# Performance work log

Measured on AMD Instinct MI355X. Metric: run time of the kernel, lower is better.

## Reference

```python
import jax, jax.numpy as jnp
import numpy as np


def _lstm_dir(xg, m, Whh, reverse):
    # xg: (T,B,4H) precomputed x@Wih.T + b ; m: (T,B) float mask
    T, B, G = xg.shape
    H = G // 4
    if reverse:
        xg = xg[::-1]
        m = m[::-1]

    def step(carry, inp):
        h, c = carry
        xg_t, m_t = inp
        gates = xg_t + h @ Whh.T
        i, f, g, o = jnp.split(gates, 4, axis=-1)  # torch gate order i,f,g,o
        i = jax.nn.sigmoid(i); f = jax.nn.sigmoid(f)
        g = jnp.tanh(g); o = jax.nn.sigmoid(o)
        c_new = f * c + i * g
        h_new = o * jnp.tanh(c_new)
        mt = m_t[:, None]
        h = mt * h_new + (1.0 - mt) * h
        c = mt * c_new + (1.0 - mt) * c
        return (h, c), h * mt  # zero outputs at padding like pad_packed_sequence

    init = (jnp.zeros((B, H), xg.dtype), jnp.zeros((B, H), xg.dtype))
    _, hs = jax.lax.scan(step, init, (xg, m))
    if reverse:
        hs = hs[::-1]
    return hs  # (T,B,H)


def _viterbi(feats, mask_f, transitions):
    # feats: (B,T,K) emissions incl. START/STOP rows; mask_f: (B,T) float
    B, T, K = feats.shape
    START, STOP = K - 2, K - 1
    part0 = transitions[START][None, :] + feats[:, 0, :]  # (B,K)
    ident = jnp.broadcast_to(jnp.arange(K)[None, :], (B, K))

    def step(part, inp):
        feat_t, m_t = inp
        cur = part[:, :, None] + transitions[None, :, :] + feat_t[:, None, :]
        new = cur.max(axis=1)
        bp = cur.argmax(axis=1)
        mb = (m_t > 0)[:, None]
        part = jnp.where(mb, new, part)        # carry partition through padding
        bp = jnp.where(mb, bp, ident)          # identity pointer at padding
        return part, bp

    part, bps = jax.lax.scan(
        step, part0, (feats[:, 1:].transpose(1, 0, 2), mask_f[:, 1:].T))
    final = part + transitions[:, STOP][None, :]
    best_score = final.max(axis=-1)            # (B,)
    last_tag = final.argmax(axis=-1)           # (B,)

    def back(tag, bp_t):
        prev = jnp.take_along_axis(bp_t, tag[:, None], axis=1)[:, 0]
        return prev, prev

    _, prevs = jax.lax.scan(back, last_tag, bps, reverse=True)  # (T-1,B)
    decode = jnp.concatenate([prevs, last_tag[None, :]], axis=0).T  # (B,T)
    return best_score, decode


def setup_inputs() -> dict:
    key = jax.random.key(0)
    ks = jax.random.split(key, 16)
    B, T, E, H = 256, 200, 256, 256
    Vc, Vf, n_labels = 10000, 100, 50
    K = n_labels + 2
    lengths = jnp.sort(jax.random.randint(ks[0], (B,), 1, T + 1))[::-1]
    lengths = lengths.at[0].set(T)
    mask = jnp.arange(T)[None, :] < lengths[:, None]
    s = 0.1
    trans = s * jax.random.normal(ks[11], (K, K), jnp.float32)
    trans = trans.at[:, K - 2].set(-10000.0)  # nothing transitions to START
    trans = trans.at[K - 1, :].set(-10000.0)  # nothing transitions from STOP
    return {
        'batch_input': jax.random.randint(ks[1], (B, T), 0, Vc),
        'batch_feature': jax.random.randint(ks[2], (B, T), 0, Vf),
        'batch_len': lengths,
        'batch_recover': jnp.arange(B),
        'mask': mask,
        'char_table': s * jax.random.normal(ks[3], (Vc, E), jnp.float32),
        'feat_table': 1.0 + s * jax.random.normal(ks[4], (Vf, E), jnp.float32),
        'Wih_f': s * jax.random.normal(ks[5], (4 * H, E), jnp.float32),
        'Whh_f': s * jax.random.normal(ks[6], (4 * H, H), jnp.float32),
        'b_f': s * jax.random.normal(ks[7], (4 * H,), jnp.float32),
        'Wih_b': s * jax.random.normal(ks[8], (4 * H, E), jnp.float32),
        'Whh_b': s * jax.random.normal(ks[9], (4 * H, H), jnp.float32),
        'b_b': s * jax.random.normal(ks[10], (4 * H,), jnp.float32),
        'W_tag': s * jax.random.normal(ks[12], (K, 2 * H), jnp.float32),
        'b_tag': s * jax.random.normal(ks[13], (K,), jnp.float32),
        'transitions': trans,
    }


def reference(batch_input, batch_feature, batch_len, batch_recover, mask,
              char_table, feat_table, Wih_f, Whh_f, b_f, Wih_b, Whh_b, b_b,
              W_tag, b_tag, transitions):
    # embeddings (dropout is identity at inference)
    emb = char_table[batch_input] * feat_table[batch_feature]  # (B,T,E)
    x = emb.transpose(1, 0, 2)                                 # (T,B,E)
    m = mask.astype(x.dtype).T                                 # (T,B)
    xg_f = jnp.einsum('tbe,ge->tbg', x, Wih_f) + b_f
    xg_b = jnp.einsum('tbe,ge->tbg', x, Wih_b) + b_b
    h_f = _lstm_dir(xg_f, m, Whh_f, reverse=False)
    h_b = _lstm_dir(xg_b, m, Whh_b, reverse=True)
    lstm_out = jnp.concatenate([h_f, h_b], axis=-1).transpose(1, 0, 2)  # (B,T,2H)
    feats = jnp.einsum('bth,kh->btk', lstm_out, W_tag) + b_tag          # (B,T,K)
    best_score, decode = _viterbi(feats, mask.astype(feats.dtype), transitions)
    decode = decode * mask.astype(decode.dtype)
    return best_score, decode
```

## Files before the change

kernel.cpp:

```cpp
#include <hip/hip_runtime.h>
#include <math.h>

#define T_ 200
#define WROW 284
#define SMEM_FLOATS (128 * WROW + 16 * WROW)
#define SMEM_BYTES (SMEM_FLOATS * 4)

typedef float f32x2 __attribute__((ext_vector_type(2)));

__device__ __forceinline__ float fsig(float x) {
  return 1.f / (1.f + __expf(-x));
}
__device__ __forceinline__ float ftanh(float x) {
  return 1.f - 2.f / (__expf(2.f * x) + 1.f);
}

__global__ __launch_bounds__(256) void xg_gemm(
    const int* __restrict__ bin, const int* __restrict__ bfe,
    const int* __restrict__ blen,
    const float* __restrict__ ctab, const float* __restrict__ ftab,
    const float* __restrict__ wih, const float* __restrict__ bias,
    float* __restrict__ xgslot, int t0, int sgn) {
  const int m0 = blockIdx.x * 128;
  const int rloc = m0 >> 8;
  const int t_blk = t0 + sgn * rloc;
  if (t_blk >= blen[m0 & 255]) return;

  __shared__ float As[32][140];
  __shared__ float Bs[32][132];
  const int tid = threadIdx.x;
  const int n0 = blockIdx.y * 128;
  const int mm = tid & 15;
  const int nn = tid >> 4;

  const int ra = tid & 127;
  const int ka = (tid >> 7) << 4;

  const int bcol = (m0 + ra) & 255;
  const float* cr = ctab + ((size_t)bin[bcol * T_ + t_blk] << 8);
  const float* fr = ftab + ((size_t)bfe[bcol * T_ + t_blk] << 8);
  const float* br = wih + (size_t)(n0 + ra) * 256;
  const int cwa = ra + ((ra >> 5) << 2);

  f32x2 acc[8][4];
  #pragma unroll
  for (int i = 0; i < 8; ++i)
    #pragma unroll
    for (int j = 0; j < 4; ++j) acc[i][j] = (f32x2){0.f, 0.f};

  const int am0 = mm * 8 + ((mm >> 2) << 2);
  const int bn0 = nn * 8;

  for (int ks = 0; ks < 256; ks += 32) {
    float4 c4[4], f4v[4], b4[4];
    #pragma unroll
    for (int w = 0; w < 4; ++w) {
      c4[w]  = *(const float4*)(cr + ks + ka + w * 4);
      f4v[w] = *(const float4*)(fr + ks + ka + w * 4);
      b4[w]  = *(const float4*)(br + ks + ka + w * 4);
    }
    __syncthreads();
    #pragma unroll
    for (int w = 0; w < 4; ++w) {
      int kk = ka + w * 4;
      As[kk + 0][cwa] = c4[w].x * f4v[w].x;
      As[kk + 1][cwa] = c4[w].y * f4v[w].y;
      As[kk + 2][cwa] = c4[w].z * f4v[w].z;
      As[kk + 3][cwa] = c4[w].w * f4v[w].w;
      Bs[kk + 0][ra] = b4[w].x;
      Bs[kk + 1][ra] = b4[w].y;
      Bs[kk + 2][ra] = b4[w].z;
      Bs[kk + 3][ra] = b4[w].w;
    }
    __syncthreads();
    #pragma unroll 4
    for (int k = 0; k < 32; ++k) {
      float4 a0 = *(const float4*)&As[k][am0];
      float4 a1 = *(const float4*)&As[k][am0 + 4];
      float4 b0 = *(const float4*)&Bs[k][bn0];
      float4 b1 = *(const float4*)&Bs[k][bn0 + 4];
      float am[8] = {a0.x, a0.y, a0.z, a0.w, a1.x, a1.y, a1.z, a1.w};
      f32x2 bp[4] = {{b0.x, b0.y}, {b0.z, b0.w}, {b1.x, b1.y}, {b1.z, b1.w}};
      #pragma unroll
      for (int i = 0; i < 8; ++i) {
        f32x2 av = {am[i], am[i]};
        #pragma unroll
        for (int j = 0; j < 4; ++j)
          acc[i][j] = __builtin_elementwise_fma(av, bp[j], acc[i][j]);
      }
    }
  }

  float4 bv0 = *(const float4*)(bias + n0 + bn0);
  float4 bv1 = *(const float4*)(bias + n0 + bn0 + 4);
  #pragma unroll
  for (int i = 0; i < 8; ++i) {
    int row = m0 + mm * 8 + i;
    float4 o0, o1;
    o0.x = acc[i][0].x + bv0.x; o0.y = acc[i][0].y + bv0.y;
    o0.z = acc[i][1].x + bv0.z; o0.w = acc[i][1].y + bv0.w;
    o1.x = acc[i][2].x + bv1.x; o1.y = acc[i][2].y + bv1.y;
    o1.z = acc[i][3].x + bv1.z; o1.w = acc[i][3].y + bv1.w;
    *(float4*)(xgslot + (size_t)row * 1024 + n0 + bn0) = o0;
    *(float4*)(xgslot + (size_t)row * 1024 + n0 + bn0 + 4) = o1;
  }
}

__global__ __launch_bounds__(512, 1) void lstm_chunk(
    const float* __restrict__ xgf, const float* __restrict__ xgb,
    const float* __restrict__ whf, const float* __restrict__ whb,
    const int* __restrict__ blen,
    float* __restrict__ hst, float* __restrict__ cst,
    float* __restrict__ hout, unsigned* __restrict__ bar,
    int s0, int nsteps) {
  extern __shared__ float smem[];
  float* wlds = smem;
  float* hlds = smem + 128 * WROW;

  const int bc = blockIdx.x, js = blockIdx.y, dir = blockIdx.z;
  const int tid = threadIdx.x;
  const int ks = tid & 7;
  const int bg = (tid >> 3) & 3;
  const int rg = tid >> 5;
  const int grp = dir * 16 + bc;
  const float* wh = dir ? whb : whf;
  const float* xgp = dir ? xgb : xgf;

  #pragma unroll
  for (int i = 0; i < 16; ++i) {
    int f = tid + i * 512;
    int prow = f >> 6;
    int k = (f & 63) << 2;
    int g = (prow >> 1) & 3, u = prow & 1, rgs = prow >> 3;
    int jg = js * 32 + rgs * 2 + u;
    float4 v = *(const float4*)(wh + ((size_t)(g * 256 + jg)) * 256 + k);
    *(float4*)&wlds[prow * WROW + k + ((k >> 5) << 2)] = v;
  }

  const int bl_th = bg * 4 + (ks & 3);
  const int b_th = bc * 16 + bl_th;
  const int u_th = ks >> 2;
  const int jth = js * 32 + rg * 2 + u_th;
  const int cjth = jth + ((jth >> 5) << 2);
  const int len_th = blen[b_th];
  float c0 = cst[((size_t)dir * 256 + b_th) * 256 + jth];

  float xq[4];
  #pragma unroll
  for (int g = 0; g < 4; ++g)
    xq[g] = xgp[(size_t)b_th * 1024 + g * 256 + jth];

  __syncthreads();

  for (int r = 0; r < nsteps; ++r) {
    const int s = s0 + r;
    const int tt = dir ? (199 - s) : s;
    const int rslot = s & 1, wslot = 1 - rslot;

    const float* hsrc = hst + (((size_t)(rslot * 2 + dir)) * 256 + bc * 16) * 256;
    {
      const int f0 = tid, f1 = tid + 512;
      const int b0i = f0 >> 6, k0 = (f0 & 63) << 2;
      const int b1i = f1 >> 6, k1 = (f1 & 63) << 2;
      const float* p0 = hsrc + (b0i << 8) + k0;
      const float* p1 = hsrc + (b1i << 8) + k1;
      float4 v0, v1;
      asm volatile(
          "global_load_dwordx4 %0, %2, off sc1\n\t"
          "global_load_dwordx4 %1, %3, off sc1\n\t"
          "s_waitcnt vmcnt(0)"
          : "=&v"(v0), "=&v"(v1)
          : "v"(p0), "v"(p1)
          : "memory");
      *(float4*)&hlds[b0i * WROW + k0 + ((k0 >> 5) << 2)] = v0;
      *(float4*)&hlds[b1i * WROW + k1 + ((k1 >> 5) << 2)] = v1;
    }
    __syncthreads();

    float xqn[4];
    const int rn = (r + 1 < nsteps) ? (r + 1) : r;
    #pragma unroll
    for (int g = 0; g < 4; ++g)
      xqn[g] = xgp[((size_t)rn * 256 + b_th) * 1024 + g * 256 + jth];

    f32x2 acc2[8][4];
    #pragma unroll
    for (int i = 0; i < 8; ++i)
      #pragma unroll
      for (int bb = 0; bb < 4; ++bb) acc2[i][bb] = (f32x2){0.f, 0.f};

    #pragma unroll
    for (int kq = 0; kq < 8; ++kq) {
      const int col = ks * 36 + kq * 4;
      float4 h4[4];
      #pragma unroll
      for (int bb = 0; bb < 4; ++bb)
        h4[bb] = *(const float4*)&hlds[(bg * 4 + bb) * WROW + col];
      f32x2 hlo[4], hhi[4];
      #pragma unroll
      for (int bb = 0; bb < 4; ++bb) {
        hlo[bb] = (f32x2){h4[bb].x, h4[bb].y};
        hhi[bb] = (f32x2){h4[bb].z, h4[bb].w};
      }
      #pragma unroll
      for (int i = 0; i < 8; ++i) {
        float4 w4 = *(const float4*)&wlds[(rg * 8 + i) * WROW + col];
        f32x2 wlo = (f32x2){w4.x, w4.y};
        f32x2 whi = (f32x2){w4.z, w4.w};
        #pragma unroll
        for (int bb = 0; bb < 4; ++bb) {
          acc2[i][bb] = __builtin_elementwise_fma(wlo, hlo[bb], acc2[i][bb]);
          acc2[i][bb] = __builtin_elementwise_fma(whi, hhi[bb], acc2[i][bb]);
        }
      }
    }

    float acc[8][4];
    #pragma unroll
    for (int i = 0; i < 8; ++i)
      #pragma unroll
      for (int bb = 0; bb < 4; ++bb)
        acc[i][bb] = acc2[i][bb].x + acc2[i][bb].y;

    const int bit0 = ks & 1, bit1 = (ks >> 1) & 1;
    float fin[8];
    #pragma unroll
    for (int i = 0; i < 8; ++i) {
      float k0 = bit0 ? acc[i][1] : acc[i][0];
      float s0v = bit0 ? acc[i][0] : acc[i][1];
      float k1 = bit0 ? acc[i][3] : acc[i][2];
      float s1v = bit0 ? acc[i][2] : acc[i][3];
      float r0 = k0 + __shfl_xor(s0v, 1);
      float r1 = k1 + __shfl_xor(s1v, 1);
      float k2 = bit1 ? r1 : r0;
      float s2v = bit1 ? r0 : r1;
      float r2 = k2 + __shfl_xor(s2v, 2);
      fin[i] = r2 + __shfl_xor(r2, 4);
    }

    float gi = fsig((u_th ? fin[1] : fin[0]) + xq[0]);
    float gf = fsig((u_th ? fin[3] : fin[2]) + xq[1]);
    float gg = ftanh((u_th ? fin[5] : fin[4]) + xq[2]);
    float go = fsig((u_th ? fin[7] : fin[6]) + xq[3]);
    float cn = gf * c0 + gi * gg;
    float hn = go * ftanh(cn);
    const bool mk = tt < len_th;
    if (mk) c0 = cn;
    float hold = hlds[bl_th * WROW + cjth];
    float hsv = mk ? hn : hold;
    __hip_atomic_store(
        hst + (((size_t)(wslot * 2 + dir)) * 256 + b_th) * 256 + jth,
        hsv, __ATOMIC_RELAXED, __HIP_MEMORY_SCOPE_AGENT);

    asm volatile("s_waitcnt vmcnt(0)" ::: "memory");
    __syncthreads();
    if (tid == 0)
      __hip_atomic_fetch_add(&bar[grp * 32], 1u, __ATOMIC_RELAXED,
                             __HIP_MEMORY_SCOPE_AGENT);
    hout[(((size_t)dir * 200 + tt) * 256 + b_th) * 256 + jth] = mk ? hn : 0.f;
    if (tid == 0) {
      const unsigned tgt = 8u * (unsigned)(s + 1);
      while (__hip_atomic_load(&bar[grp * 32], __ATOMIC_RELAXED,
                               __HIP_MEMORY_SCOPE_AGENT) < tgt) {}
    }
    __syncthreads();

    #pragma unroll
    for (int g = 0; g < 4; ++g) xq[g] = xqn[g];
  }

  cst[((size_t)dir * 256 + b_th) * 256 + jth] = c0;
}

__global__ __launch_bounds__(256) void feats_kernel(
    const float* __restrict__ h_out, const float* __restrict__ wtag,
    const float* __restrict__ btag, float* __restrict__ feats) {
  __shared__ float hcat[32][512];
  const int t = blockIdx.x, bc = blockIdx.y;
  const int tid = threadIdx.x;
  const float* hf = h_out + (((size_t)0 * 200 + t) * 256 + bc * 32) * 256;
  const float* hb = h_out + (((size_t)1 * 200 + t) * 256 + bc * 32) * 256;
  for (int i = tid; i < 2048; i += 256) {
    int row = i >> 6, c4 = (i & 63) << 2;
    *(float4*)&hcat[row][c4] = *(const float4*)(hf + (size_t)row * 256 + c4);
    *(float4*)&hcat[row][256 + c4] = *(const float4*)(hb + (size_t)row * 256 + c4);
  }
  __syncthreads();
  const int kk = tid & 63;
  const int bg = tid >> 6;
  if (kk < 52) {
    f32x2 acc2[8];
    #pragma unroll
    for (int i = 0; i < 8; ++i) acc2[i] = (f32x2){0.f, 0.f};
    const float* wr = wtag + (size_t)kk * 512;
    for (int jq = 0; jq < 128; ++jq) {
      float4 wv = *(const float4*)(wr + jq * 4);
      f32x2 wlo = (f32x2){wv.x, wv.y};
      f32x2 whi = (f32x2){wv.z, wv.w};
      #pragma unroll
      for (int bi = 0; bi < 8; ++bi) {
        float4 hv = *(const float4*)&hcat[bg * 8 + bi][jq * 4];
        f32x2 hlo = (f32x2){hv.x, hv.y};
        f32x2 hhi = (f32x2){hv.z, hv.w};
        acc2[bi] = __builtin_elementwise_fma(wlo, hlo, acc2[bi]);
        acc2[bi] = __builtin_elementwise_fma(whi, hhi, acc2[bi]);
      }
    }
    float bv = btag[kk];
    #pragma unroll
    for (int bi = 0; bi < 8; ++bi)
      feats[(size_t)(bc * 32 + bg * 8 + bi) * 10400 + t * 52 + kk] =
          acc2[bi].x + acc2[bi].y + bv;
  }
}

__global__ __launch_bounds__(64) void viterbi_kernel(
    const float* __restrict__ feats, const float* __restrict__ trans,
    const int* __restrict__ blen, float* __restrict__ out) {
  __shared__ float flds[10400];
  __shared__ float pl[56];
  __shared__ unsigned char bp[199 * 52];

  const int b = blockIdx.x;
  const int lane = threadIdx.x;
  const int kk = (lane < 52) ? lane : 0;
  const float* fb = feats + (size_t)b * 10400;
  const int len = blen[b];

  for (int i = lane; i < 2600; i += 64)
    *(float4*)&flds[i * 4] = *(const float4*)(fb + i * 4);

  float trc[52];
  #pragma unroll
  for (int j = 0; j < 52; ++j) trc[j] = trans[j * 52 + kk];
  __syncthreads();

  float part = trans[50 * 52 + kk] + flds[kk];
  if (lane < 52) pl[lane] = part;

  for (int t = 1; t < 200; ++t) {
    const float ftk = flds[t * 52 + kk];
    float pa[52];
    #pragma unroll
    for (int q = 0; q < 13; ++q) {
      float4 v = *(const float4*)&pl[q * 4];
      pa[q * 4 + 0] = v.x; pa[q * 4 + 1] = v.y;
      pa[q * 4 + 2] = v.z; pa[q * 4 + 3] = v.w;
    }
    float mv0 = -1e30f, mv1 = -1e30f, mv2 = -1e30f, mv3 = -1e30f;
    int mj0 = 0, mj1 = 13, mj2 = 26, mj3 = 39;
    #pragma unroll
    for (int q = 0; q < 13; ++q) {
      float c0v = (pa[q] + trc[q]) + ftk;
      if (c0v > mv0) { mv0 = c0v; mj0 = q; }
      float c1v = (pa[13 + q] + trc[13 + q]) + ftk;
      if (c1v > mv1) { mv1 = c1v; mj1 = 13 + q; }
      float c2v = (pa[26 + q] + trc[26 + q]) + ftk;
      if (c2v > mv2) { mv2 = c2v; mj2 = 26 + q; }
      float c3v = (pa[39 + q] + trc[39 + q]) + ftk;
      if (c3v > mv3) { mv3 = c3v; mj3 = 39 + q; }
    }
    float mv = mv0; int mj = mj0;
    if (mv1 > mv) { mv = mv1; mj = mj1; }
    if (mv2 > mv) { mv = mv2; mj = mj2; }
    if (mv3 > mv) { mv = mv3; mj = mj3; }
    const bool m = t < len;
    if (lane < 52) {
      bp[(t - 1) * 52 + lane] = (unsigned char)(m ? mj : lane);
      if (m) { part = mv; pl[lane] = mv; }
    }
  }

  float fin = (lane < 52) ? (part + trans[lane * 52 + 51]) : -1e30f;
  int bi = lane;
  #pragma unroll
  for (int off = 32; off; off >>= 1) {
    float ov = __shfl_down(fin, off);
    int oi = __shfl_down(bi, off);
    if (ov > fin || (ov == fin && oi < bi)) { fin = ov; bi = oi; }
  }
  if (lane == 0) {
    out[b] = fin;
    int tag = bi;
    float* dec = out + 256 + (size_t)b * 200;
    dec[199] = (199 < len) ? (float)tag : 0.f;
    for (int i = 198; i >= 0; --i) {
      tag = bp[i * 52 + tag];
      dec[i] = (i < len) ? (float)tag : 0.f;
    }
  }
}

extern "C" void kernel_launch(void* const* d_in, const int* in_sizes, int n_in,
                              void* d_out, int out_size, void* d_ws, size_t ws_size,
                              hipStream_t stream) {
  const int*   bin  = (const int*)d_in[0];
  const int*   bfe  = (const int*)d_in[1];
  const int*   blen = (const int*)d_in[2];
  const float* ctab = (const float*)d_in[5];
  const float* ftab = (const float*)d_in[6];
  const float* wihf = (const float*)d_in[7];
  const float* whhf = (const float*)d_in[8];
  const float* bf   = (const float*)d_in[9];
  const float* wihb = (const float*)d_in[10];
  const float* whhb = (const float*)d_in[11];
  const float* bb   = (const float*)d_in[12];
  const float* wtag = (const float*)d_in[13];
  const float* btag = (const float*)d_in[14];
  const float* trn  = (const float*)d_in[15];

  (void)hipFuncSetAttribute(reinterpret_cast<const void*>(lstm_chunk),
                            hipFuncAttributeMaxDynamicSharedMemorySize,
                            SMEM_BYTES);

  const size_t FIXED_F = 29271040;
  size_t ws_f = ws_size / sizeof(float);
  int C = 1;
  const int cands[10] = {50, 40, 25, 20, 10, 8, 5, 4, 2, 1};
  for (int u = 0; u < 10; ++u) {
    if (FIXED_F + (size_t)2 * cands[u] * 262144 <= ws_f) { C = cands[u]; break; }
  }

  float* ws  = (float*)d_ws;
  float* xgf = ws;
  float* xgb = xgf + (size_t)C * 262144;
  float* hst = xgb + (size_t)C * 262144;
  float* cst = hst + 262144;
  float* hout = cst + 131072;
  float* fts  = hout + 26214400;
  unsigned* bar = (unsigned*)(fts + 2662400);
  float* out  = (float*)d_out;

  hipMemsetAsync(hst, 0, (size_t)(262144 + 131072) * sizeof(float), stream);
  hipMemsetAsync(bar, 0, 1024 * sizeof(unsigned), stream);

  const int nchunks = 200 / C;
  for (int c = 0; c < nchunks; ++c) {
    xg_gemm<<<dim3(2 * C, 8), 256, 0, stream>>>(bin, bfe, blen, ctab, ftab,
                                                wihf, bf, xgf, c * C, 1);
    xg_gemm<<<dim3(2 * C, 8), 256, 0, stream>>>(bin, bfe, blen, ctab, ftab,
                                                wihb, bb, xgb, 199 - c * C, -1);
    lstm_chunk<<<dim3(16, 8, 2), 512, SMEM_BYTES, stream>>>(
        xgf, xgb, whhf, whhb, blen, hst, cst, hout, bar, c * C, C);
  }
  feats_kernel<<<dim3(200, 8), 256, 0, stream>>>(hout, wtag, btag, fts);
  viterbi_kernel<<<256, 64, 0, stream>>>(fts, trn, blen, out);
}
```

Measured before the change: 2.243 ms.

## Prefetch LSTM weights, use DPP reductions, skip padded steps in feats and Viterbi

Inside the LSTM recurrent step, the W tile loads for the next k-slice are software-pipelined into registers, and two of the cross-lane shuffles are replaced with DPP quad permutes. The feats kernel now exits early for timesteps past the first sequence length of each 32-row batch chunk. The Viterbi kernel loads only the valid prefix, runs only up to each sequence's length, and backtracks only over valid positions. Skipping feats blocks assumes lengths are sorted descending within each batch chunk, and the prefetch raises register pressure in the LSTM kernel.

```diff
diff --git a/kernel.cpp b/kernel.cpp
--- a/kernel.cpp
+++ b/kernel.cpp
@@ -13,6 +13,14 @@
 }
 __device__ __forceinline__ float ftanh(float x) {
   return 1.f - 2.f / (__expf(2.f * x) + 1.f);
+}
+__device__ __forceinline__ float dpp_xor1(float x) {
+  return __int_as_float(__builtin_amdgcn_update_dpp(
+      0, __float_as_int(x), 0xB1, 0xF, 0xF, true));
+}
+__device__ __forceinline__ float dpp_xor2(float x) {
+  return __int_as_float(__builtin_amdgcn_update_dpp(
+      0, __float_as_int(x), 0x4E, 0xF, 0xF, true));
 }
 
 __global__ __launch_bounds__(256) void xg_gemm(
@@ -189,6 +197,11 @@
       #pragma unroll
       for (int bb = 0; bb < 4; ++bb) acc2[i][bb] = (f32x2){0.f, 0.f};
 
+    float4 w4c[8];
+    #pragma unroll
+    for (int i = 0; i < 8; ++i)
+      w4c[i] = *(const float4*)&wlds[(rg * 8 + i) * WROW + ks * 36];
+
     #pragma unroll
     for (int kq = 0; kq < 8; ++kq) {
       const int col = ks * 36 + kq * 4;
@@ -196,6 +209,12 @@
       #pragma unroll
       for (int bb = 0; bb < 4; ++bb)
         h4[bb] = *(const float4*)&hlds[(bg * 4 + bb) * WROW + col];
+      float4 w4n[8];
+      if (kq < 7) {
+        #pragma unroll
+        for (int i = 0; i < 8; ++i)
+          w4n[i] = *(const float4*)&wlds[(rg * 8 + i) * WROW + col + 4];
+      }
       f32x2 hlo[4], hhi[4];
       #pragma unroll
       for (int bb = 0; bb < 4; ++bb) {
@@ -204,15 +223,18 @@
       }
       #pragma unroll
       for (int i = 0; i < 8; ++i) {
-        float4 w4 = *(const float4*)&wlds[(rg * 8 + i) * WROW + col];
-        f32x2 wlo = (f32x2){w4.x, w4.y};
-        f32x2 whi = (f32x2){w4.z, w4.w};
+        f32x2 wlo = (f32x2){w4c[i].x, w4c[i].y};
+        f32x2 whi = (f32x2){w4c[i].z, w4c[i].w};
         #pragma unroll
         for (int bb = 0; bb < 4; ++bb) {
           acc2[i][bb] = __builtin_elementwise_fma(wlo, hlo[bb], acc2[i][bb]);
           acc2[i][bb] = __builtin_elementwise_fma(whi, hhi[bb], acc2[i][bb]);
         }
       }
+      if (kq < 7) {
+        #pragma unroll
+        for (int i = 0; i < 8; ++i) w4c[i] = w4n[i];
+      }
     }
 
     float acc[8][4];
@@ -230,11 +252,11 @@
       float s0v = bit0 ? acc[i][0] : acc[i][1];
       float k1 = bit0 ? acc[i][3] : acc[i][2];
       float s1v = bit0 ? acc[i][2] : acc[i][3];
-      float r0 = k0 + __shfl_xor(s0v, 1);
-      float r1 = k1 + __shfl_xor(s1v, 1);
+      float r0 = k0 + dpp_xor1(s0v);
+      float r1 = k1 + dpp_xor1(s1v);
       float k2 = bit1 ? r1 : r0;
       float s2v = bit1 ? r0 : r1;
-      float r2 = k2 + __shfl_xor(s2v, 2);
+      float r2 = k2 + dpp_xor2(s2v);
       fin[i] = r2 + __shfl_xor(r2, 4);
     }
 
@@ -274,9 +296,11 @@
 
 __global__ __launch_bounds__(256) void feats_kernel(
     const float* __restrict__ h_out, const float* __restrict__ wtag,
-    const float* __restrict__ btag, float* __restrict__ feats) {
+    const float* __restrict__ btag, float* __restrict__ feats,
+    const int* __restrict__ blen) {
+  const int t = blockIdx.x, bc = blockIdx.y;
+  if (t >= blen[bc * 32]) return;
   __shared__ float hcat[32][512];
-  const int t = blockIdx.x, bc = blockIdx.y;
   const int tid = threadIdx.x;
   const float* hf = h_out + (((size_t)0 * 200 + t) * 256 + bc * 32) * 256;
   const float* hb = h_out + (((size_t)1 * 200 + t) * 256 + bc * 32) * 256;
@@ -327,7 +351,8 @@
   const float* fb = feats + (size_t)b * 10400;
   const int len = blen[b];
 
-  for (int i = lane; i < 2600; i += 64)
+  const int nf4 = (len * 52 + 3) >> 2;
+  for (int i = lane; i < nf4; i += 64)
     *(float4*)&flds[i * 4] = *(const float4*)(fb + i * 4);
 
   float trc[52];
@@ -338,7 +363,7 @@
   float part = trans[50 * 52 + kk] + flds[kk];
   if (lane < 52) pl[lane] = part;
 
-  for (int t = 1; t < 200; ++t) {
+  for (int t = 1; t < len; ++t) {
     const float ftk = flds[t * 52 + kk];
     float pa[52];
     #pragma unroll
@@ -364,10 +389,9 @@
     if (mv1 > mv) { mv = mv1; mj = mj1; }
     if (mv2 > mv) { mv = mv2; mj = mj2; }
     if (mv3 > mv) { mv = mv3; mj = mj3; }
-    const bool m = t < len;
     if (lane < 52) {
-      bp[(t - 1) * 52 + lane] = (unsigned char)(m ? mj : lane);
-      if (m) { part = mv; pl[lane] = mv; }
+      bp[(t - 1) * 52 + lane] = (unsigned char)mj;
+      part = mv; pl[lane] = mv;
     }
   }
 
@@ -381,12 +405,13 @@
   }
   if (lane == 0) {
     out[b] = fin;
+    float* dec = out + 256 + (size_t)b * 200;
+    for (int i = len; i < 200; ++i) dec[i] = 0.f;
     int tag = bi;
-    float* dec = out + 256 + (size_t)b * 200;
-    dec[199] = (199 < len) ? (float)tag : 0.f;
-    for (int i = 198; i >= 0; --i) {
+    dec[len - 1] = (float)tag;
+    for (int i = len - 2; i >= 0; --i) {
       tag = bp[i * 52 + tag];
-      dec[i] = (i < len) ? (float)tag : 0.f;
+      dec[i] = (float)tag;
     }
   }
 }
@@ -443,6 +468,6 @@
     lstm_chunk<<<dim3(16, 8, 2), 512, SMEM_BYTES, stream>>>(
         xgf, xgb, whhf, whhb, blen, hst, cst, hout, bar, c * C, C);
   }
-  feats_kernel<<<dim3(200, 8), 256, 0, stream>>>(hout, wtag, btag, fts);
+  feats_kernel<<<dim3(200, 8), 256, 0, stream>>>(hout, wtag, btag, fts, blen);
   viterbi_kernel<<<256, 64, 0, stream>>>(fts, trn, blen, out);
 }
```

Result: no change. 2.218 ms (-1.1%).
